# Kernel tuning notes

Measured on AMD Instinct MI355X. Metric: run time of the kernel, lower is better.

## Reference

```python
import jax, jax.numpy as jnp
import numpy as np

NORM_EPS = 1e-6
QK_SCALE = 1.0 / 128.0  # 1/d_head (muP)
ROTARY_BASE = 10000
INFTY_APPROX = 1e30

B, T, M, H, D = 2, 2048, 1024, 8, 128


def _rmsnorm(x, eps=NORM_EPS):
    # normalize over the last (head) dim; no learned gains (norm_gains=False)
    ms = jnp.mean(jnp.square(x), axis=-1, keepdims=True)
    return x / jnp.sqrt(ms + eps)


def _rope(x, base=ROTARY_BASE):
    # x: [b, h, t, d]; rotate (even-half, odd-half) pairs as in the source
    length, width = x.shape[-2], x.shape[-1]
    half = width // 2
    pos = jnp.arange(length, dtype=x.dtype)[:, None]            # [t, 1]
    freqs = jnp.power(jnp.asarray(base, x.dtype), -jnp.arange(half, dtype=x.dtype) / half)[None, :]
    rad = pos * freqs                                            # [t, half]
    cos = jnp.cos(rad)[None, None]
    sin = jnp.sin(rad)[None, None]
    even, odd = jnp.split(x, 2, axis=-1)
    return jnp.concatenate([even * cos - odd * sin, even * sin + odd * cos], axis=-1)


def setup_inputs() -> dict:
    key = jax.random.key(0)
    ks = jax.random.split(key, 5)
    std = M ** -0.5
    return {
        "x": jax.random.normal(ks[0], (B, T, M), jnp.float32),
        "wq": jax.random.normal(ks[1], (M, H, D), jnp.float32) * std,
        "wk": jax.random.normal(ks[2], (M, H, D), jnp.float32) * std,
        "wv": jax.random.normal(ks[3], (M, H, D), jnp.float32) * std,
        "wo": jax.random.normal(ks[4], (H, D, M), jnp.float32) * std,
    }


def reference(x, wq, wk, wv, wo):
    # projections: [b, h, t, d]
    q = jnp.einsum('bim,mhd->bhid', x, wq)
    k = jnp.einsum('bim,mhd->bhid', x, wk)
    v = jnp.einsum('bim,mhd->bhid', x, wv)
    # qk RMSNorm (norm_gains=False)
    q = _rmsnorm(q)
    k = _rmsnorm(k)
    # inline RoPE
    q = _rope(q)
    k = _rope(k)
    # scaled scores: mult applied to both q and k (mult^2 = qk_scale)
    mult = jnp.asarray(QK_SCALE ** 0.5, q.dtype)
    s = jnp.einsum('bhid,bhjd->bhij', q * mult, k * mult)
    # causal mask: subtract large constant where i < j
    t = s.shape[-1]
    mask = (jnp.arange(t)[:, None] < jnp.arange(t)[None, :]).astype(s.dtype)
    s = s - jnp.asarray(INFTY_APPROX, s.dtype) * mask[None, None]
    p = jax.nn.softmax(s, axis=-1)
    o = jnp.einsum('bhij,bhjd->bhid', p, v)
    return jnp.einsum('bhid,hdm->bim', o, wo)
```

## Files before the change

### kernel.cpp

```cpp
#include <hip/hip_runtime.h>
#include <hip/hip_bf16.h>
#include <math.h>

#define B_  2
#define T_  2048
#define M_  1024
#define H_  8
#define D_  128
#define NROW (B_ * T_)
#define HD  (H_ * D_)

#define NORM_EPS 1e-6f
#define QK_MULT  0.08838834764831845f
#define LN_BASE_64 0.14391156510f

typedef short bf16x8  __attribute__((ext_vector_type(8)));
typedef float f32x4   __attribute__((ext_vector_type(4)));
typedef float f32x16  __attribute__((ext_vector_type(16)));
typedef unsigned int uint32x2 __attribute__((ext_vector_type(2)));

static __device__ __forceinline__ unsigned short f2bf(float f) {
    union { __hip_bfloat16 h; unsigned short u; } cv;
    cv.h = __float2bfloat16(f);
    return cv.u;
}
static __device__ __forceinline__ float bf2f(unsigned short u) {
    union { unsigned short u; __hip_bfloat16 h; } cv;
    cv.u = u;
    return __bfloat162float(cv.h);
}
static __device__ __forceinline__ unsigned int pk2bf(float a, float b) {
    return ((unsigned int)f2bf(b) << 16) | f2bf(a);
}

static __device__ __forceinline__ void gload_lds16(const unsigned short* g,
                                                   unsigned short* l) {
    __builtin_amdgcn_global_load_lds(
        (const __attribute__((address_space(1))) void*)g,
        (__attribute__((address_space(3))) void*)l, 16, 0, 0);
}

__global__ __launch_bounds__(256) void prep(const float* __restrict__ x,
                                            const float* __restrict__ w0,
                                            const float* __restrict__ w1,
                                            const float* __restrict__ w2,
                                            const float* __restrict__ w3,
                                            unsigned short* __restrict__ xb,
                                            unsigned short* __restrict__ wqkvT,
                                            unsigned short* __restrict__ woT)
{
    __shared__ float t[32][33];
    const int z = blockIdx.z;
    if (z == 4) {
        const size_t base = ((size_t)blockIdx.y * 32 + blockIdx.x) * 4096;
        #pragma unroll
        for (int it = 0; it < 4; ++it) {
            const size_t i = base + it * 1024 + threadIdx.x * 4;
            const float4 v = *(const float4*)(x + i);
            ushort4 o;
            o.x = f2bf(v.x); o.y = f2bf(v.y); o.z = f2bf(v.z); o.w = f2bf(v.w);
            *(ushort4*)(xb + i) = o;
        }
        return;
    }
    const float* in = z == 0 ? w0 : (z == 1 ? w1 : (z == 2 ? w2 : w3));
    unsigned short* out = z < 3 ? (wqkvT + (size_t)z * 1024 * 1024) : woT;

    const int tx = threadIdx.x & 31;
    const int ty = threadIdx.x >> 5;
    const int n0 = blockIdx.x * 32;
    const int k0 = blockIdx.y * 32;
    #pragma unroll
    for (int r = 0; r < 4; ++r)
        t[ty + r * 8][tx] = in[(size_t)(k0 + ty + r * 8) * 1024 + n0 + tx];
    __syncthreads();
    #pragma unroll
    for (int r = 0; r < 4; ++r)
        out[(size_t)(n0 + ty + r * 8) * 1024 + k0 + tx] = f2bf(t[tx][ty + r * 8]);
}

__global__ __launch_bounds__(256) void gemm_qkv(const unsigned short* __restrict__ A,
                                                const unsigned short* __restrict__ Bt,
                                                unsigned short* __restrict__ oq,
                                                unsigned short* __restrict__ ok,
                                                unsigned short* __restrict__ vt)
{
    __shared__ unsigned short As[2][128 * 32];
    __shared__ unsigned short Bs[2][128 * 32];

    const int tid  = threadIdx.x;
    const int lane = tid & 63;
    const int w    = tid >> 6;
    const int g    = lane >> 4;
    const int lc   = lane & 15;

    const int m0 = blockIdx.y * 128;
    const int n0 = blockIdx.x * 128;

    const unsigned short* aBase = A  + (size_t)m0 * 1024;
    const unsigned short* bBase = Bt + (size_t)n0 * 1024;

    int dstOff[2];
    size_t srcOff[2];
    #pragma unroll
    for (int it = 0; it < 2; ++it) {
        const int u  = tid + it * 256;
        const int r2 = u >> 2;
        const int sg = (u & 3) ^ (r2 & 3);
        dstOff[it] = u * 8;
        srcOff[it] = (size_t)r2 * 1024 + sg * 8;
    }

    f32x4 acc[2][8];
    #pragma unroll
    for (int i = 0; i < 2; ++i)
        #pragma unroll
        for (int j = 0; j < 8; ++j)
            acc[i][j] = (f32x4){0.f, 0.f, 0.f, 0.f};

    #pragma unroll
    for (int it = 0; it < 2; ++it) {
        gload_lds16(aBase + srcOff[it], &As[0][dstOff[it]]);
        gload_lds16(bBase + srcOff[it], &Bs[0][dstOff[it]]);
    }

    for (int kt = 0; kt < 32; ++kt) {
        const int cur = kt & 1;
        __syncthreads();

        if (kt < 31) {
            const int k0n = (kt + 1) * 32;
            #pragma unroll
            for (int it = 0; it < 2; ++it) {
                gload_lds16(aBase + srcOff[it] + k0n, &As[cur ^ 1][dstOff[it]]);
                gload_lds16(bBase + srcOff[it] + k0n, &Bs[cur ^ 1][dstOff[it]]);
            }
        }

        const int sw = (g ^ (lc & 3)) << 3;
        bf16x8 af[2], bfr[8];
        #pragma unroll
        for (int i = 0; i < 2; ++i)
            af[i] = *(const bf16x8*)&As[cur][(w * 32 + i * 16 + lc) * 32 + sw];
        #pragma unroll
        for (int j = 0; j < 8; ++j)
            bfr[j] = *(const bf16x8*)&Bs[cur][(j * 16 + lc) * 32 + sw];

        #pragma unroll
        for (int i = 0; i < 2; ++i)
            #pragma unroll
            for (int j = 0; j < 8; ++j)
                acc[i][j] = __builtin_amdgcn_mfma_f32_16x16x32_bf16(af[i], bfr[j], acc[i][j], 0, 0, 0);
    }

    const int which = n0 >> 10;
    const int ncol0 = n0 & 1023;
    if (which < 2) {
        unsigned short* outp = which == 0 ? oq : ok;
        float freq[4];
        #pragma unroll
        for (int j = 0; j < 4; ++j)
            freq[j] = __expf(-(float)(j * 16 + lc) * LN_BASE_64);

        #pragma unroll
        for (int i = 0; i < 2; ++i)
            #pragma unroll
            for (int r = 0; r < 4; ++r) {
                float s = 0.f;
                #pragma unroll
                for (int j = 0; j < 8; ++j) s += acc[i][j][r] * acc[i][j][r];
                #pragma unroll
                for (int off = 1; off < 16; off <<= 1) s += __shfl_xor(s, off);
                const float rms = rsqrtf(s * (1.0f / 128.0f) + NORM_EPS) * QK_MULT;

                const int trow = m0 + w * 32 + i * 16 + g * 4 + r;
                const float tpos = (float)(trow & (T_ - 1));
                unsigned short* op = outp + (size_t)trow * 1024 + ncol0;
                #pragma unroll
                for (int j = 0; j < 4; ++j) {
                    float sn, cs;
                    __sincosf(tpos * freq[j], &sn, &cs);
                    const float e = acc[i][j][r] * rms;
                    const float o = acc[i][j + 4][r] * rms;
                    op[j * 16 + lc]      = f2bf(e * cs - o * sn);
                    op[j * 16 + lc + 64] = f2bf(e * sn + o * cs);
                }
            }
    } else {
        const int b2 = m0 >> 11;
        const int hh = ncol0 >> 7;
        #pragma unroll
        for (int i = 0; i < 2; ++i) {
            const int t = (m0 & 2047) + w * 32 + i * 16 + g * 4;
            #pragma unroll
            for (int j = 0; j < 8; ++j) {
                const int dd = j * 16 + lc;
                uint2 val;
                val.x = pk2bf(acc[i][j][0], acc[i][j][1]);
                val.y = pk2bf(acc[i][j][2], acc[i][j][3]);
                *(uint2*)(vt + (((size_t)(b2 * 8 + hh) * 128 + dd) * T_ + t)) = val;
            }
        }
    }
}

__global__ __launch_bounds__(256) void gemm_out(const unsigned short* __restrict__ A,
                                                const unsigned short* __restrict__ Bt,
                                                float* __restrict__ cf)
{
    __shared__ unsigned short As[2][128 * 64];
    __shared__ unsigned short Bs[2][64 * 64];

    const int tid  = threadIdx.x;
    const int lane = tid & 63;
    const int w    = tid >> 6;
    const int g    = lane >> 4;
    const int lc   = lane & 15;
    const int wm   = w >> 1;
    const int wn   = w & 1;

    const int m0 = blockIdx.y * 128;
    const int n0 = blockIdx.x * 64;

    const unsigned short* aBase = A  + (size_t)m0 * 1024;
    const unsigned short* bBase = Bt + (size_t)n0 * 1024;

    int dstA[4], dstB[2];
    size_t srcA[4], srcB[2];
    #pragma unroll
    for (int it = 0; it < 4; ++it) {
        const int u  = tid + it * 256;
        const int r2 = u >> 3;
        const int sg = (u & 7) ^ (r2 & 7);
        dstA[it] = u * 8;
        srcA[it] = (size_t)r2 * 1024 + sg * 8;
    }
    #pragma unroll
    for (int it = 0; it < 2; ++it) {
        const int u  = tid + it * 256;
        const int r2 = u >> 3;
        const int sg = (u & 7) ^ (r2 & 7);
        dstB[it] = u * 8;
        srcB[it] = (size_t)r2 * 1024 + sg * 8;
    }

    f32x4 acc[4][2];
    #pragma unroll
    for (int i = 0; i < 4; ++i)
        #pragma unroll
        for (int j = 0; j < 2; ++j)
            acc[i][j] = (f32x4){0.f, 0.f, 0.f, 0.f};

    #pragma unroll
    for (int it = 0; it < 4; ++it)
        gload_lds16(aBase + srcA[it], &As[0][dstA[it]]);
    #pragma unroll
    for (int it = 0; it < 2; ++it)
        gload_lds16(bBase + srcB[it], &Bs[0][dstB[it]]);

    for (int kt = 0; kt < 16; ++kt) {
        const int cur = kt & 1;
        __syncthreads();

        if (kt < 15) {
            const int k0n = (kt + 1) * 64;
            #pragma unroll
            for (int it = 0; it < 4; ++it)
                gload_lds16(aBase + srcA[it] + k0n, &As[cur ^ 1][dstA[it]]);
            #pragma unroll
            for (int it = 0; it < 2; ++it)
                gload_lds16(bBase + srcB[it] + k0n, &Bs[cur ^ 1][dstB[it]]);
        }

        #pragma unroll
        for (int dc = 0; dc < 2; ++dc) {
            const int sw = ((dc * 4 + g) ^ (lc & 7)) << 3;
            bf16x8 af[4], bfr[2];
            #pragma unroll
            for (int i = 0; i < 4; ++i)
                af[i] = *(const bf16x8*)&As[cur][(wm * 64 + i * 16 + lc) * 64 + sw];
            #pragma unroll
            for (int j = 0; j < 2; ++j)
                bfr[j] = *(const bf16x8*)&Bs[cur][(wn * 32 + j * 16 + lc) * 64 + sw];

            #pragma unroll
            for (int i = 0; i < 4; ++i)
                #pragma unroll
                for (int j = 0; j < 2; ++j)
                    acc[i][j] = __builtin_amdgcn_mfma_f32_16x16x32_bf16(af[i], bfr[j], acc[i][j], 0, 0, 0);
        }
    }

    #pragma unroll
    for (int i = 0; i < 4; ++i) {
        const int mrow = m0 + wm * 64 + i * 16 + g * 4;
        #pragma unroll
        for (int j = 0; j < 2; ++j) {
            const int nc = n0 + wn * 32 + j * 16 + lc;
            #pragma unroll
            for (int r = 0; r < 4; ++r)
                cf[(size_t)(mrow + r) * 1024 + nc] = acc[i][j][r];
        }
    }
}

__global__ __launch_bounds__(256) void flash_attn(const unsigned short* __restrict__ qb,
                                                  const unsigned short* __restrict__ kb,
                                                  const unsigned short* __restrict__ vt,
                                                  unsigned short* __restrict__ o)
{
    __shared__ __align__(16) unsigned short smem[2 * 64 * 128 + 2 * 128 * 64 + 128];
    unsigned short* KsB = smem;
    unsigned short* VsB = smem + 2 * 64 * 128;
    float* lscr = (float*)(smem + 2 * 64 * 128 + 2 * 128 * 64);
    float* scr  = (float*)smem;

    const int tid  = threadIdx.x;
    const int lane = tid & 63;
    const int w    = tid >> 6;
    const int wj   = w >> 1;
    const int wq2  = w & 1;
    const int qcol = lane & 31;
    const int hi   = lane >> 5;

    const int bh = blockIdx.x;
    const int h  = bh & (H_ - 1);
    const int b  = bh >> 3;
    const int yy = blockIdx.y;
    const int qt = yy < 16 ? yy : 47 - yy;
    const int q0 = qt * 64;

    const size_t bhbase  = (size_t)b * T_ * HD + (size_t)h * 128;
    const size_t bhvbase = (size_t)bh * 128 * T_;

    int mI[4];
    size_t srcKoff[4], srcVoff[4];
    #pragma unroll
    for (int it = 0; it < 4; ++it) {
        const int m = (w * 4 + it) * 64 + lane;
        mI[it] = m;
        const int jK = m >> 4, cK = (m & 15) ^ (jK & 15);
        srcKoff[it] = (size_t)jK * 1024 + cK * 8;
        const int dV = m >> 3, cV = (m & 7) ^ (dV & 7);
        srcVoff[it] = (size_t)dV * T_ + cV * 8;
    }
    const unsigned short* kgb = kb + bhbase;
    const unsigned short* vgb = vt + bhvbase;

    bf16x8 qf[8];
    {
        const unsigned short* qp = qb + bhbase + (size_t)(q0 + wq2 * 32 + qcol) * 1024 + hi * 8;
        #pragma unroll
        for (int ks = 0; ks < 8; ++ks)
            qf[ks] = *(const bf16x8*)(qp + ks * 16);
    }

    float lsum = 0.f;
    f32x16 otacc[4];
    #pragma unroll
    for (int dch = 0; dch < 4; ++dch)
        #pragma unroll
        for (int r = 0; r < 16; ++r) otacc[dch][r] = 0.f;

    #pragma unroll
    for (int it = 0; it < 4; ++it) {
        gload_lds16(kgb + srcKoff[it], &KsB[mI[it] * 8]);
        gload_lds16(vgb + srcVoff[it], &VsB[mI[it] * 8]);
    }

    for (int jt = 0; jt <= qt; ++jt) {
        const int cur = jt & 1;
        unsigned short* Ks = KsB + cur * (64 * 128);
        unsigned short* Vs = VsB + cur * (128 * 64);
        __syncthreads();

        if (jt < qt) {
            const size_t j0n = (size_t)(jt + 1) * 64;
            unsigned short* Kn = KsB + (cur ^ 1) * (64 * 128);
            unsigned short* Vn = VsB + (cur ^ 1) * (128 * 64);
            #pragma unroll
            for (int it = 0; it < 4; ++it) {
                gload_lds16(kgb + j0n * 1024 + srcKoff[it], &Kn[mI[it] * 8]);
                gload_lds16(vgb + j0n + srcVoff[it], &Vn[mI[it] * 8]);
            }
        }

        const bool dead = (jt == qt) && (wj > wq2);
        if (!dead) {
            const int jrow = wj * 32 + qcol;

            bf16x8 kf[8], vf[8];
            #pragma unroll
            for (int ks = 0; ks < 8; ++ks) {
                const int c = ks * 2 + hi;
                kf[ks] = *(const bf16x8*)&Ks[(jrow * 16 + (c ^ (lane & 15))) * 8];
            }
            #pragma unroll
            for (int ks2 = 0; ks2 < 2; ++ks2)
                #pragma unroll
                for (int dch = 0; dch < 4; ++dch) {
                    const int c = wj * 4 + ks2 * 2 + hi;
                    const int drow = dch * 32 + qcol;
                    vf[ks2 * 4 + dch] = *(const bf16x8*)&Vs[(drow * 8 + (c ^ (lane & 7))) * 8];
                }

            f32x16 sacc0, sacc1;
            #pragma unroll
            for (int r = 0; r < 16; ++r) { sacc0[r] = 0.f; sacc1[r] = 0.f; }
            __builtin_amdgcn_s_setprio(1);
            #pragma unroll
            for (int ks = 0; ks < 8; ks += 2) {
                sacc0 = __builtin_amdgcn_mfma_f32_32x32x16_bf16(kf[ks], qf[ks], sacc0, 0, 0, 0);
                sacc1 = __builtin_amdgcn_mfma_f32_32x32x16_bf16(kf[ks + 1], qf[ks + 1], sacc1, 0, 0, 0);
            }
            __builtin_amdgcn_s_setprio(0);
            f32x16 sacc = sacc0 + sacc1;

            if (jt == qt && wj == wq2) {
                #pragma unroll
                for (int r = 0; r < 16; ++r) {
                    const int jl = (r & 3) + 8 * (r >> 2) + 4 * hi;
                    if (qcol < jl) sacc[r] = -1e30f;
                }
            }

            unsigned int dw[8];
            #pragma unroll
            for (int m2 = 0; m2 < 8; ++m2) {
                const float p0 = __expf(sacc[2 * m2]);
                const float p1 = __expf(sacc[2 * m2 + 1]);
                lsum += p0 + p1;
                dw[m2] = pk2bf(p0, p1);
            }

            __builtin_amdgcn_s_setprio(1);
            #pragma unroll
            for (int ks2 = 0; ks2 < 2; ++ks2) {
                const uint32x2 s02 = __builtin_amdgcn_permlane32_swap(
                    dw[4 * ks2 + 0], dw[4 * ks2 + 2], 0, 0);
                const uint32x2 s13 = __builtin_amdgcn_permlane32_swap(
                    dw[4 * ks2 + 1], dw[4 * ks2 + 3], 0, 0);
                union { unsigned int u[4]; bf16x8 v; } pf;
                pf.u[0] = s02[0];
                pf.u[1] = s13[0];
                pf.u[2] = s02[1];
                pf.u[3] = s13[1];
                #pragma unroll
                for (int dch = 0; dch < 4; ++dch)
                    otacc[dch] = __builtin_amdgcn_mfma_f32_32x32x16_bf16(vf[ks2 * 4 + dch], pf.v, otacc[dch], 0, 0, 0);
            }
            __builtin_amdgcn_s_setprio(0);
        }
    }

    lsum += __shfl_xor(lsum, 32);
    __syncthreads();

    if (wj == 1) {
        float* s0 = scr + (size_t)(wq2 * 32 + qcol) * 129;
        #pragma unroll
        for (int dch = 0; dch < 4; ++dch)
            #pragma unroll
            for (int r = 0; r < 16; ++r)
                s0[dch * 32 + (r & 3) + 8 * (r >> 2) + 4 * hi] = otacc[dch][r];
        if (hi == 0) lscr[wq2 * 32 + qcol] = lsum;
    }
    __syncthreads();
    if (wj == 0) {
        const float l = lsum + lscr[wq2 * 32 + qcol];
        const float inv = 1.0f / l;
        const float* s0 = scr + (size_t)(wq2 * 32 + qcol) * 129;
        unsigned short* op = o + bhbase + (size_t)(q0 + wq2 * 32 + qcol) * 1024;
        #pragma unroll
        for (int dch = 0; dch < 4; ++dch) {
            #pragma unroll
            for (int k4 = 0; k4 < 4; ++k4) {
                const int d0 = dch * 32 + 8 * k4 + 4 * hi;
                const float f0 = (otacc[dch][4 * k4 + 0] + s0[d0 + 0]) * inv;
                const float f1 = (otacc[dch][4 * k4 + 1] + s0[d0 + 1]) * inv;
                const float f2 = (otacc[dch][4 * k4 + 2] + s0[d0 + 2]) * inv;
                const float f3 = (otacc[dch][4 * k4 + 3] + s0[d0 + 3]) * inv;
                uint2 val;
                val.x = pk2bf(f0, f1);
                val.y = pk2bf(f2, f3);
                *(uint2*)(op + d0) = val;
            }
        }
    }
}

extern "C" void kernel_launch(void* const* d_in, const int* in_sizes, int n_in,
                              void* d_out, int out_size, void* d_ws, size_t ws_size,
                              hipStream_t stream)
{
    const float* x  = (const float*)d_in[0];
    const float* wq = (const float*)d_in[1];
    const float* wk = (const float*)d_in[2];
    const float* wv = (const float*)d_in[3];
    const float* wo = (const float*)d_in[4];
    float* out = (float*)d_out;

    const size_t SZ = (size_t)NROW * HD;
    unsigned short* qb    = (unsigned short*)d_ws;
    unsigned short* kb    = qb + SZ;
    unsigned short* vt    = kb + SZ;
    unsigned short* ob    = vt + SZ;
    unsigned short* xb    = ob + SZ;
    unsigned short* wqkvT = xb + SZ;
    unsigned short* woT   = wqkvT + 3 * 1024 * 1024;

    prep<<<dim3(32, 32, 5), 256, 0, stream>>>(x, wq, wk, wv, wo, xb, wqkvT, woT);

    gemm_qkv<<<dim3(24, 32), 256, 0, stream>>>(xb, wqkvT, qb, kb, vt);

    flash_attn<<<dim3(B_ * H_, 32), 256, 0, stream>>>(qb, kb, vt, ob);

    gemm_out<<<dim3(16, 32), 256, 0, stream>>>(ob, woT, out);
}
```

Measured before the change: 180.5 us.

## Use atomic work-queue scheduling in flash attention and stage V transpose through LDS

Flash attention becomes a persistent-style kernel: 512 blocks pull (q-tile, batch-head) units from per-group atomic counters, handing out the longest causal tiles first to balance load. The counters sit in the output buffer, are zeroed by prep, and are later overwritten by gemm_out. The V-transposed epilogue of the QKV GEMM now stages the tile in shared memory and writes coalesced 16-byte rows instead of scattered 8-byte stores. The cost is atomic traffic, extra barriers and a reliance on output-buffer scratch ordering.

```diff
diff --git a/kernel.cpp b/kernel.cpp
--- a/kernel.cpp
+++ b/kernel.cpp
@@ -24,11 +24,6 @@
     cv.h = __float2bfloat16(f);
     return cv.u;
 }
-static __device__ __forceinline__ float bf2f(unsigned short u) {
-    union { unsigned short u; __hip_bfloat16 h; } cv;
-    cv.u = u;
-    return __bfloat162float(cv.h);
-}
 static __device__ __forceinline__ unsigned int pk2bf(float a, float b) {
     return ((unsigned int)f2bf(b) << 16) | f2bf(a);
 }
@@ -47,11 +42,14 @@
                                             const float* __restrict__ w3,
                                             unsigned short* __restrict__ xb,
                                             unsigned short* __restrict__ wqkvT,
-                                            unsigned short* __restrict__ woT)
+                                            unsigned short* __restrict__ woT,
+                                            int* __restrict__ ctr)
 {
     __shared__ float t[32][33];
     const int z = blockIdx.z;
     if (z == 4) {
+        if (blockIdx.x == 0 && blockIdx.y == 0 && threadIdx.x < 8)
+            ctr[threadIdx.x] = 0;
         const size_t base = ((size_t)blockIdx.y * 32 + blockIdx.x) * 4096;
         #pragma unroll
         for (int it = 0; it < 4; ++it) {
@@ -85,8 +83,9 @@
                                                 unsigned short* __restrict__ ok,
                                                 unsigned short* __restrict__ vt)
 {
-    __shared__ unsigned short As[2][128 * 32];
-    __shared__ unsigned short Bs[2][128 * 32];
+    __shared__ __align__(16) unsigned short smem[17408];
+    #define AsQ(buf) (smem + (buf) * 4096)
+    #define BsQ(buf) (smem + 8192 + (buf) * 4096)
 
     const int tid  = threadIdx.x;
     const int lane = tid & 63;
@@ -120,8 +119,8 @@
 
     #pragma unroll
     for (int it = 0; it < 2; ++it) {
-        gload_lds16(aBase + srcOff[it], &As[0][dstOff[it]]);
-        gload_lds16(bBase + srcOff[it], &Bs[0][dstOff[it]]);
+        gload_lds16(aBase + srcOff[it], AsQ(0) + dstOff[it]);
+        gload_lds16(bBase + srcOff[it], BsQ(0) + dstOff[it]);
     }
 
     for (int kt = 0; kt < 32; ++kt) {
@@ -132,8 +131,8 @@
             const int k0n = (kt + 1) * 32;
             #pragma unroll
             for (int it = 0; it < 2; ++it) {
-                gload_lds16(aBase + srcOff[it] + k0n, &As[cur ^ 1][dstOff[it]]);
-                gload_lds16(bBase + srcOff[it] + k0n, &Bs[cur ^ 1][dstOff[it]]);
+                gload_lds16(aBase + srcOff[it] + k0n, AsQ(cur ^ 1) + dstOff[it]);
+                gload_lds16(bBase + srcOff[it] + k0n, BsQ(cur ^ 1) + dstOff[it]);
             }
         }
 
@@ -141,10 +140,10 @@
         bf16x8 af[2], bfr[8];
         #pragma unroll
         for (int i = 0; i < 2; ++i)
-            af[i] = *(const bf16x8*)&As[cur][(w * 32 + i * 16 + lc) * 32 + sw];
+            af[i] = *(const bf16x8*)&AsQ(cur)[(w * 32 + i * 16 + lc) * 32 + sw];
         #pragma unroll
         for (int j = 0; j < 8; ++j)
-            bfr[j] = *(const bf16x8*)&Bs[cur][(j * 16 + lc) * 32 + sw];
+            bfr[j] = *(const bf16x8*)&BsQ(cur)[(j * 16 + lc) * 32 + sw];
 
         #pragma unroll
         for (int i = 0; i < 2; ++i)
@@ -189,19 +188,31 @@
     } else {
         const int b2 = m0 >> 11;
         const int hh = ncol0 >> 7;
+        const int PAD = 136;
+        __syncthreads();
         #pragma unroll
         for (int i = 0; i < 2; ++i) {
-            const int t = (m0 & 2047) + w * 32 + i * 16 + g * 4;
+            const int t0 = w * 32 + i * 16 + g * 4;
             #pragma unroll
             for (int j = 0; j < 8; ++j) {
-                const int dd = j * 16 + lc;
                 uint2 val;
                 val.x = pk2bf(acc[i][j][0], acc[i][j][1]);
                 val.y = pk2bf(acc[i][j][2], acc[i][j][3]);
-                *(uint2*)(vt + (((size_t)(b2 * 8 + hh) * 128 + dd) * T_ + t)) = val;
+                *(uint2*)&smem[(j * 16 + lc) * PAD + t0] = val;
             }
         }
-    }
+        __syncthreads();
+        const int row  = tid >> 1;
+        const int half = tid & 1;
+        const unsigned short* src = &smem[row * PAD + half * 64];
+        unsigned short* dst = vt + ((size_t)(b2 * 8 + hh) * 128 + row) * T_
+                                 + (m0 & 2047) + half * 64;
+        #pragma unroll
+        for (int it2 = 0; it2 < 8; ++it2)
+            *(uint4*)(dst + it2 * 8) = *(const uint4*)(src + it2 * 8);
+    }
+    #undef AsQ
+    #undef BsQ
 }
 
 __global__ __launch_bounds__(256) void gemm_out(const unsigned short* __restrict__ A,
@@ -307,9 +318,11 @@
 __global__ __launch_bounds__(256) void flash_attn(const unsigned short* __restrict__ qb,
                                                   const unsigned short* __restrict__ kb,
                                                   const unsigned short* __restrict__ vt,
-                                                  unsigned short* __restrict__ o)
+                                                  unsigned short* __restrict__ o,
+                                                  int* __restrict__ ctr)
 {
     __shared__ __align__(16) unsigned short smem[2 * 64 * 128 + 2 * 128 * 64 + 128];
+    __shared__ int unitLds;
     unsigned short* KsB = smem;
     unsigned short* VsB = smem + 2 * 64 * 128;
     float* lscr = (float*)(smem + 2 * 64 * 128 + 2 * 128 * 64);
@@ -323,15 +336,7 @@
     const int qcol = lane & 31;
     const int hi   = lane >> 5;
 
-    const int bh = blockIdx.x;
-    const int h  = bh & (H_ - 1);
-    const int b  = bh >> 3;
-    const int yy = blockIdx.y;
-    const int qt = yy < 16 ? yy : 47 - yy;
-    const int q0 = qt * 64;
-
-    const size_t bhbase  = (size_t)b * T_ * HD + (size_t)h * 128;
-    const size_t bhvbase = (size_t)bh * 128 * T_;
+    const int p = blockIdx.x & 7;
 
     int mI[4];
     size_t srcKoff[4], srcVoff[4];
@@ -344,148 +349,164 @@
         const int dV = m >> 3, cV = (m & 7) ^ (dV & 7);
         srcVoff[it] = (size_t)dV * T_ + cV * 8;
     }
-    const unsigned short* kgb = kb + bhbase;
-    const unsigned short* vgb = vt + bhvbase;
-
-    bf16x8 qf[8];
-    {
-        const unsigned short* qp = qb + bhbase + (size_t)(q0 + wq2 * 32 + qcol) * 1024 + hi * 8;
-        #pragma unroll
-        for (int ks = 0; ks < 8; ++ks)
-            qf[ks] = *(const bf16x8*)(qp + ks * 16);
-    }
-
-    float lsum = 0.f;
-    f32x16 otacc[4];
-    #pragma unroll
-    for (int dch = 0; dch < 4; ++dch)
-        #pragma unroll
-        for (int r = 0; r < 16; ++r) otacc[dch][r] = 0.f;
-
-    #pragma unroll
-    for (int it = 0; it < 4; ++it) {
-        gload_lds16(kgb + srcKoff[it], &KsB[mI[it] * 8]);
-        gload_lds16(vgb + srcVoff[it], &VsB[mI[it] * 8]);
-    }
-
-    for (int jt = 0; jt <= qt; ++jt) {
-        const int cur = jt & 1;
-        unsigned short* Ks = KsB + cur * (64 * 128);
-        unsigned short* Vs = VsB + cur * (128 * 64);
-        __syncthreads();
-
-        if (jt < qt) {
-            const size_t j0n = (size_t)(jt + 1) * 64;
-            unsigned short* Kn = KsB + (cur ^ 1) * (64 * 128);
-            unsigned short* Vn = VsB + (cur ^ 1) * (128 * 64);
-            #pragma unroll
-            for (int it = 0; it < 4; ++it) {
-                gload_lds16(kgb + j0n * 1024 + srcKoff[it], &Kn[mI[it] * 8]);
-                gload_lds16(vgb + j0n + srcVoff[it], &Vn[mI[it] * 8]);
+
+    for (;;) {
+        if (tid == 0) unitLds = atomicAdd(&ctr[p], 1);
+        __syncthreads();
+        const int u = unitLds;
+        if (u >= 64) break;
+        const int qt = 31 - (u >> 1);
+        const int bh = p + 8 * (u & 1);
+        const int q0 = qt * 64;
+        const int h  = bh & (H_ - 1);
+        const int b  = bh >> 3;
+
+        const size_t bhbase  = (size_t)b * T_ * HD + (size_t)h * 128;
+        const size_t bhvbase = (size_t)bh * 128 * T_;
+        const unsigned short* kgb = kb + bhbase;
+        const unsigned short* vgb = vt + bhvbase;
+
+        bf16x8 qf[8];
+        {
+            const unsigned short* qp = qb + bhbase + (size_t)(q0 + wq2 * 32 + qcol) * 1024 + hi * 8;
+            #pragma unroll
+            for (int ks = 0; ks < 8; ++ks)
+                qf[ks] = *(const bf16x8*)(qp + ks * 16);
+        }
+
+        float lsum = 0.f;
+        f32x16 otacc[4];
+        #pragma unroll
+        for (int dch = 0; dch < 4; ++dch)
+            #pragma unroll
+            for (int r = 0; r < 16; ++r) otacc[dch][r] = 0.f;
+
+        #pragma unroll
+        for (int it = 0; it < 4; ++it) {
+            gload_lds16(kgb + srcKoff[it], &KsB[mI[it] * 8]);
+            gload_lds16(vgb + srcVoff[it], &VsB[mI[it] * 8]);
+        }
+
+        for (int jt = 0; jt <= qt; ++jt) {
+            const int cur = jt & 1;
+            unsigned short* Ks = KsB + cur * (64 * 128);
+            unsigned short* Vs = VsB + cur * (128 * 64);
+            __syncthreads();
+
+            if (jt < qt) {
+                const size_t j0n = (size_t)(jt + 1) * 64;
+                unsigned short* Kn = KsB + (cur ^ 1) * (64 * 128);
+                unsigned short* Vn = VsB + (cur ^ 1) * (128 * 64);
+                #pragma unroll
+                for (int it = 0; it < 4; ++it) {
+                    gload_lds16(kgb + j0n * 1024 + srcKoff[it], &Kn[mI[it] * 8]);
+                    gload_lds16(vgb + j0n + srcVoff[it], &Vn[mI[it] * 8]);
+                }
             }
-        }
-
-        const bool dead = (jt == qt) && (wj > wq2);
-        if (!dead) {
-            const int jrow = wj * 32 + qcol;
-
-            bf16x8 kf[8], vf[8];
-            #pragma unroll
-            for (int ks = 0; ks < 8; ++ks) {
-                const int c = ks * 2 + hi;
-                kf[ks] = *(const bf16x8*)&Ks[(jrow * 16 + (c ^ (lane & 15))) * 8];
+
+            const bool dead = (jt == qt) && (wj > wq2);
+            if (!dead) {
+                const int jrow = wj * 32 + qcol;
+
+                bf16x8 kf[8], vf[8];
+                #pragma unroll
+                for (int ks = 0; ks < 8; ++ks) {
+                    const int c = ks * 2 + hi;
+                    kf[ks] = *(const bf16x8*)&Ks[(jrow * 16 + (c ^ (lane & 15))) * 8];
+                }
+                #pragma unroll
+                for (int ks2 = 0; ks2 < 2; ++ks2)
+                    #pragma unroll
+                    for (int dch = 0; dch < 4; ++dch) {
+                        const int c = wj * 4 + ks2 * 2 + hi;
+                        const int drow = dch * 32 + qcol;
+                        vf[ks2 * 4 + dch] = *(const bf16x8*)&Vs[(drow * 8 + (c ^ (lane & 7))) * 8];
+                    }
+
+                f32x16 sacc0, sacc1;
+                #pragma unroll
+                for (int r = 0; r < 16; ++r) { sacc0[r] = 0.f; sacc1[r] = 0.f; }
+                __builtin_amdgcn_s_setprio(1);
+                #pragma unroll
+                for (int ks = 0; ks < 8; ks += 2) {
+                    sacc0 = __builtin_amdgcn_mfma_f32_32x32x16_bf16(kf[ks], qf[ks], sacc0, 0, 0, 0);
+                    sacc1 = __builtin_amdgcn_mfma_f32_32x32x16_bf16(kf[ks + 1], qf[ks + 1], sacc1, 0, 0, 0);
+                }
+                __builtin_amdgcn_s_setprio(0);
+                f32x16 sacc = sacc0 + sacc1;
+
+                if (jt == qt && wj == wq2) {
+                    #pragma unroll
+                    for (int r = 0; r < 16; ++r) {
+                        const int jl = (r & 3) + 8 * (r >> 2) + 4 * hi;
+                        if (qcol < jl) sacc[r] = -1e30f;
+                    }
+                }
+
+                unsigned int dw[8];
+                #pragma unroll
+                for (int m2 = 0; m2 < 8; ++m2) {
+                    const float p0 = __expf(sacc[2 * m2]);
+                    const float p1 = __expf(sacc[2 * m2 + 1]);
+                    lsum += p0 + p1;
+                    dw[m2] = pk2bf(p0, p1);
+                }
+
+                __builtin_amdgcn_s_setprio(1);
+                #pragma unroll
+                for (int ks2 = 0; ks2 < 2; ++ks2) {
+                    const uint32x2 s02 = __builtin_amdgcn_permlane32_swap(
+                        dw[4 * ks2 + 0], dw[4 * ks2 + 2], 0, 0);
+                    const uint32x2 s13 = __builtin_amdgcn_permlane32_swap(
+                        dw[4 * ks2 + 1], dw[4 * ks2 + 3], 0, 0);
+                    union { unsigned int u2[4]; bf16x8 v; } pf;
+                    pf.u2[0] = s02[0];
+                    pf.u2[1] = s13[0];
+                    pf.u2[2] = s02[1];
+                    pf.u2[3] = s13[1];
+                    #pragma unroll
+                    for (int dch = 0; dch < 4; ++dch)
+                        otacc[dch] = __builtin_amdgcn_mfma_f32_32x32x16_bf16(vf[ks2 * 4 + dch], pf.v, otacc[dch], 0, 0, 0);
+                }
+                __builtin_amdgcn_s_setprio(0);
             }
-            #pragma unroll
-            for (int ks2 = 0; ks2 < 2; ++ks2)
-                #pragma unroll
-                for (int dch = 0; dch < 4; ++dch) {
-                    const int c = wj * 4 + ks2 * 2 + hi;
-                    const int drow = dch * 32 + qcol;
-                    vf[ks2 * 4 + dch] = *(const bf16x8*)&Vs[(drow * 8 + (c ^ (lane & 7))) * 8];
-                }
-
-            f32x16 sacc0, sacc1;
-            #pragma unroll
-            for (int r = 0; r < 16; ++r) { sacc0[r] = 0.f; sacc1[r] = 0.f; }
-            __builtin_amdgcn_s_setprio(1);
-            #pragma unroll
-            for (int ks = 0; ks < 8; ks += 2) {
-                sacc0 = __builtin_amdgcn_mfma_f32_32x32x16_bf16(kf[ks], qf[ks], sacc0, 0, 0, 0);
-                sacc1 = __builtin_amdgcn_mfma_f32_32x32x16_bf16(kf[ks + 1], qf[ks + 1], sacc1, 0, 0, 0);
+        }
+
+        lsum += __shfl_xor(lsum, 32);
+        __syncthreads();
+
+        if (wj == 1) {
+            float* s0 = scr + (size_t)(wq2 * 32 + qcol) * 129;
+            #pragma unroll
+            for (int dch = 0; dch < 4; ++dch)
+                #pragma unroll
+                for (int r = 0; r < 16; ++r)
+                    s0[dch * 32 + (r & 3) + 8 * (r >> 2) + 4 * hi] = otacc[dch][r];
+            if (hi == 0) lscr[wq2 * 32 + qcol] = lsum;
+        }
+        __syncthreads();
+        if (wj == 0) {
+            const float l = lsum + lscr[wq2 * 32 + qcol];
+            const float inv = 1.0f / l;
+            const float* s0 = scr + (size_t)(wq2 * 32 + qcol) * 129;
+            unsigned short* op = o + bhbase + (size_t)(q0 + wq2 * 32 + qcol) * 1024;
+            #pragma unroll
+            for (int dch = 0; dch < 4; ++dch) {
+                #pragma unroll
+                for (int k4 = 0; k4 < 4; ++k4) {
+                    const int d0 = dch * 32 + 8 * k4 + 4 * hi;
+                    const float f0 = (otacc[dch][4 * k4 + 0] + s0[d0 + 0]) * inv;
+                    const float f1 = (otacc[dch][4 * k4 + 1] + s0[d0 + 1]) * inv;
+                    const float f2 = (otacc[dch][4 * k4 + 2] + s0[d0 + 2]) * inv;
+                    const float f3 = (otacc[dch][4 * k4 + 3] + s0[d0 + 3]) * inv;
+                    uint2 val;
+                    val.x = pk2bf(f0, f1);
+                    val.y = pk2bf(f2, f3);
+                    *(uint2*)(op + d0) = val;
+                }
             }
-            __builtin_amdgcn_s_setprio(0);
-            f32x16 sacc = sacc0 + sacc1;
-
-            if (jt == qt && wj == wq2) {
-                #pragma unroll
-                for (int r = 0; r < 16; ++r) {
-                    const int jl = (r & 3) + 8 * (r >> 2) + 4 * hi;
-                    if (qcol < jl) sacc[r] = -1e30f;
-                }
-            }
-
-            unsigned int dw[8];
-            #pragma unroll
-            for (int m2 = 0; m2 < 8; ++m2) {
-                const float p0 = __expf(sacc[2 * m2]);
-                const float p1 = __expf(sacc[2 * m2 + 1]);
-                lsum += p0 + p1;
-                dw[m2] = pk2bf(p0, p1);
-            }
-
-            __builtin_amdgcn_s_setprio(1);
-            #pragma unroll
-            for (int ks2 = 0; ks2 < 2; ++ks2) {
-                const uint32x2 s02 = __builtin_amdgcn_permlane32_swap(
-                    dw[4 * ks2 + 0], dw[4 * ks2 + 2], 0, 0);
-                const uint32x2 s13 = __builtin_amdgcn_permlane32_swap(
-                    dw[4 * ks2 + 1], dw[4 * ks2 + 3], 0, 0);
-                union { unsigned int u[4]; bf16x8 v; } pf;
-                pf.u[0] = s02[0];
-                pf.u[1] = s13[0];
-                pf.u[2] = s02[1];
-                pf.u[3] = s13[1];
-                #pragma unroll
-                for (int dch = 0; dch < 4; ++dch)
-                    otacc[dch] = __builtin_amdgcn_mfma_f32_32x32x16_bf16(vf[ks2 * 4 + dch], pf.v, otacc[dch], 0, 0, 0);
-            }
-            __builtin_amdgcn_s_setprio(0);
-        }
-    }
-
-    lsum += __shfl_xor(lsum, 32);
-    __syncthreads();
-
-    if (wj == 1) {
-        float* s0 = scr + (size_t)(wq2 * 32 + qcol) * 129;
-        #pragma unroll
-        for (int dch = 0; dch < 4; ++dch)
-            #pragma unroll
-            for (int r = 0; r < 16; ++r)
-                s0[dch * 32 + (r & 3) + 8 * (r >> 2) + 4 * hi] = otacc[dch][r];
-        if (hi == 0) lscr[wq2 * 32 + qcol] = lsum;
-    }
-    __syncthreads();
-    if (wj == 0) {
-        const float l = lsum + lscr[wq2 * 32 + qcol];
-        const float inv = 1.0f / l;
-        const float* s0 = scr + (size_t)(wq2 * 32 + qcol) * 129;
-        unsigned short* op = o + bhbase + (size_t)(q0 + wq2 * 32 + qcol) * 1024;
-        #pragma unroll
-        for (int dch = 0; dch < 4; ++dch) {
-            #pragma unroll
-            for (int k4 = 0; k4 < 4; ++k4) {
-                const int d0 = dch * 32 + 8 * k4 + 4 * hi;
-                const float f0 = (otacc[dch][4 * k4 + 0] + s0[d0 + 0]) * inv;
-                const float f1 = (otacc[dch][4 * k4 + 1] + s0[d0 + 1]) * inv;
-                const float f2 = (otacc[dch][4 * k4 + 2] + s0[d0 + 2]) * inv;
-                const float f3 = (otacc[dch][4 * k4 + 3] + s0[d0 + 3]) * inv;
-                uint2 val;
-                val.x = pk2bf(f0, f1);
-                val.y = pk2bf(f2, f3);
-                *(uint2*)(op + d0) = val;
-            }
-        }
+        }
+        __syncthreads();
     }
 }
 
@@ -508,12 +529,13 @@
     unsigned short* xb    = ob + SZ;
     unsigned short* wqkvT = xb + SZ;
     unsigned short* woT   = wqkvT + 3 * 1024 * 1024;
-
-    prep<<<dim3(32, 32, 5), 256, 0, stream>>>(x, wq, wk, wv, wo, xb, wqkvT, woT);
+    int* ctr = (int*)out;
+
+    prep<<<dim3(32, 32, 5), 256, 0, stream>>>(x, wq, wk, wv, wo, xb, wqkvT, woT, ctr);
 
     gemm_qkv<<<dim3(24, 32), 256, 0, stream>>>(xb, wqkvT, qb, kb, vt);
 
-    flash_attn<<<dim3(B_ * H_, 32), 256, 0, stream>>>(qb, kb, vt, ob);
+    flash_attn<<<dim3(512), 256, 0, stream>>>(qb, kb, vt, ob, ctr);
 
     gemm_out<<<dim3(16, 32), 256, 0, stream>>>(ob, woT, out);
 }
```

Measured after the change: 193.1 us. 1.07x slower.
